# Optimization experiments

Measured on AMD Instinct MI355X. Metric: run time of the kernel, lower is better.

Reference implementation:

```python
import jax, jax.numpy as jnp
import numpy as np

B, S, L = 4, 1024, 512          # batch, max_seqlen, actual per-seq length
H, D = 12, 64                   # heads, head_dim
DIM = H * D                     # 768
NNZ = B * L                     # 2048 unpadded tokens


def setup_inputs() -> dict:
    key = jax.random.key(0)
    k1, k2, k3 = jax.random.split(key, 3)
    hidden_states = jax.random.normal(k1, (NNZ, DIM), jnp.float32)
    Wqkv_w = jax.random.normal(k2, (3 * DIM, DIM), jnp.float32) * 0.02
    Wqkv_b = jnp.zeros((3 * DIM,), jnp.float32)
    # ALiBi-style bias; in the real model it also encodes the padding mask (-inf),
    # here random values suffice for a correctness baseline.
    bias = jax.random.normal(k3, (B, H, S, S), jnp.float32) * 0.1
    # each sequence occupies the first L slots of its row in the padded layout
    indices = (jnp.arange(B)[:, None] * S + jnp.arange(L)[None, :]).reshape(-1).astype(jnp.int32)
    cu_seqlens = (jnp.arange(B + 1) * L).astype(jnp.int32)
    attn_mask = jnp.zeros((B, S), jnp.int32).at[:, :L].set(1)
    return dict(hidden_states=hidden_states, Wqkv_w=Wqkv_w, Wqkv_b=Wqkv_b,
                bias=bias, indices=indices, attn_mask=attn_mask,
                cu_seqlens=cu_seqlens, max_seqlen_in_batch=S)


def reference(hidden_states, Wqkv_w, Wqkv_b, bias, indices, attn_mask,
              cu_seqlens, max_seqlen_in_batch):
    b = attn_mask.shape[0]
    s = max_seqlen_in_batch
    # QKV projection on unpadded tokens: (nnz, 3*dim)
    qkv = hidden_states @ Wqkv_w.T + Wqkv_b
    # pad_input: scatter unpadded rows into (b*s) padded layout
    padded = jnp.zeros((b * s, qkv.shape[-1]), qkv.dtype).at[indices].set(qkv)
    qkv = padded.reshape(b, s, 3, H, D)
    q, k, v = qkv[:, :, 0], qkv[:, :, 1], qkv[:, :, 2]  # (b, s, h, d)
    scale = 1.0 / float(np.sqrt(D))
    scores = jnp.einsum('bqhd,bkhd->bhqk', q, k) * scale + bias  # (b,h,s,s)
    probs = jax.nn.softmax(scores, axis=-1)
    ctx = jnp.einsum('bhqk,bkhd->bqhd', probs, v)  # (b, s, h, d)
    # unpad_input_only: gather back rows where attn_mask == 1 (== indices)
    return ctx.reshape(b * s, H * D)[indices]
```

## Files before the change

kernel.cpp:

```cpp
#include <hip/hip_runtime.h>
#include <hip/hip_bf16.h>
#include <cstdint>

typedef short  s16x8 __attribute__((ext_vector_type(8)));
typedef ushort u16x8 __attribute__((ext_vector_type(8)));
typedef ushort u16x4 __attribute__((ext_vector_type(4)));
typedef float  f32x4 __attribute__((ext_vector_type(4)));

#define B_    4
#define S_    1024
#define H_    12
#define D_    64
#define DIM_  768
#define QSCALE 0.18033688011112042f
#define LOG2E  1.4426950408889634f

#define NTAIL 384
#define NGEMM 576

__device__ __forceinline__ ushort f2bf(float f) {
    __bf16 h = (__bf16)f;
    return __builtin_bit_cast(ushort, h);
}

__device__ __forceinline__ u16x8 cvt8(f32x4 x, f32x4 y) {
    u16x8 r;
    r[0]=f2bf(x[0]); r[1]=f2bf(x[1]); r[2]=f2bf(x[2]); r[3]=f2bf(x[3]);
    r[4]=f2bf(y[0]); r[5]=f2bf(y[1]); r[6]=f2bf(y[2]); r[7]=f2bf(y[3]);
    return r;
}

__global__ __launch_bounds__(256) void gemm_tail(
    const float* __restrict__ hidden, const float* __restrict__ W,
    const float* __restrict__ bvec, const float* __restrict__ bias,
    const int* __restrict__ cu,
    ushort* __restrict__ Qu, ushort* __restrict__ Ku, ushort* __restrict__ Vt,
    float* __restrict__ T, int nrows, int nnz)
{
    const int t = threadIdx.x;

    if ((int)blockIdx.x >= NGEMM) {
        const int blk = blockIdx.x - NGEMM;
        const int w = t >> 6, l = t & 63, grp = l >> 4, lc = l & 15;
        for (int rid = blk*16 + w*4 + grp; rid < nrows; rid += NTAIL*16) {
            const int h = rid / nnz;
            const int u = rid - h * nnz;
            int b = 0;
            while (cu[b+1] <= u) b++;
            const int q  = u - cu[b];
            const int Lb = cu[b+1] - cu[b];
            const float* rp = bias + ((size_t)(b*H_ + h)*S_ + q)*S_;
            float s = 0.0f;
            for (int kbase = Lb; kbase < S_; kbase += 512) {
                f32x4 v[8];
                #pragma unroll
                for (int i = 0; i < 8; i++) {
                    const int k = kbase + lc*4 + i*64;
                    v[i] = (k < S_) ? *(const f32x4*)(rp + k) : (f32x4)(-1e30f);
                }
                #pragma unroll
                for (int i = 0; i < 8; i++)
                    s += exp2f(v[i][0]*LOG2E) + exp2f(v[i][1]*LOG2E)
                       + exp2f(v[i][2]*LOG2E) + exp2f(v[i][3]*LOG2E);
            }
            s += __shfl_xor(s, 1, 64);
            s += __shfl_xor(s, 2, 64);
            s += __shfl_xor(s, 4, 64);
            s += __shfl_xor(s, 8, 64);
            if (lc == 0) T[(size_t)(b*H_ + h)*S_ + q] = s;
        }
        return;
    }

    const int bid = ((int)blockIdx.x % 8) * (NGEMM/8) + (int)blockIdx.x / 8;

    __shared__ ushort As[128][40];
    __shared__ ushort Bs[64][40];

    const int n0 = (bid % 36) * 64;
    const int m0 = (bid / 36) * 128;
    const int w  = t >> 6, l = t & 63, lg = l >> 4, lc = l & 15;

    const int srow = t >> 1, shalf = t & 1;
    const int brow = t >> 2, bq = t & 3;
    const float* aSrc = hidden + (size_t)(m0 + srow) * DIM_ + shalf * 16;
    const float* bSrc = W      + (size_t)(n0 + brow) * DIM_ + bq * 8;

    f32x4 acc[2][4];
    #pragma unroll
    for (int i = 0; i < 2; i++)
        #pragma unroll
        for (int j = 0; j < 4; j++) acc[i][j] = (f32x4)0.0f;

    for (int k0 = 0; k0 < DIM_; k0 += 32) {
        __syncthreads();
        {
            const f32x4* a4 = (const f32x4*)(aSrc + k0);
            f32x4 x0 = a4[0], x1 = a4[1], x2 = a4[2], x3 = a4[3];
            const f32x4* b4 = (const f32x4*)(bSrc + k0);
            f32x4 y0 = b4[0], y1 = b4[1];
            *(u16x8*)&As[srow][shalf*16]     = cvt8(x0, x1);
            *(u16x8*)&As[srow][shalf*16 + 8] = cvt8(x2, x3);
            *(u16x8*)&Bs[brow][bq*8]         = cvt8(y0, y1);
        }
        __syncthreads();
        s16x8 af[2], bfr[4];
        #pragma unroll
        for (int mi = 0; mi < 2; mi++)
            af[mi] = *(const s16x8*)&As[w*32 + mi*16 + lc][lg*8];
        #pragma unroll
        for (int ni = 0; ni < 4; ni++)
            bfr[ni] = *(const s16x8*)&Bs[ni*16 + lc][lg*8];
        #pragma unroll
        for (int mi = 0; mi < 2; mi++)
            #pragma unroll
            for (int ni = 0; ni < 4; ni++)
                acc[mi][ni] = __builtin_amdgcn_mfma_f32_16x16x32_bf16(
                                  af[mi], bfr[ni], acc[mi][ni], 0, 0, 0);
    }

    const int sec = n0 / DIM_;
    float bv[4];
    #pragma unroll
    for (int ni = 0; ni < 4; ni++) bv[ni] = bvec[n0 + ni*16 + lc];

    #pragma unroll
    for (int mi = 0; mi < 2; mi++) {
        const int r = m0 + w*32 + mi*16 + lg*4;
        if (sec == 2) {
            int b = 0;
            while (cu[b+1] <= r) b++;
            const int q = r - cu[b];
            #pragma unroll
            for (int ni = 0; ni < 4; ni++) {
                const int nl = (n0 - 2*DIM_) + ni*16 + lc;
                const int h = nl >> 6, d = nl & 63;
                u16x4 pk;
                #pragma unroll
                for (int j = 0; j < 4; j++) pk[j] = f2bf(acc[mi][ni][j] + bv[ni]);
                *(u16x4*)&Vt[((size_t)((b*H_ + h)*64 + d))*S_ + q] = pk;
            }
        } else {
            #pragma unroll
            for (int j = 0; j < 4; j++) {
                #pragma unroll
                for (int ni = 0; ni < 4; ni++) {
                    const int nl = (n0 - sec*DIM_) + ni*16 + lc;
                    float v = acc[mi][ni][j] + bv[ni];
                    if (sec == 0) Qu[(size_t)(r+j)*DIM_ + nl] = f2bf(v * QSCALE);
                    else          Ku[(size_t)(r+j)*DIM_ + nl] = f2bf(v);
                }
            }
        }
    }
}

__global__ __launch_bounds__(128) void attn_kernel(
    const ushort* __restrict__ Qu, const ushort* __restrict__ Ku,
    const ushort* __restrict__ Vt, const float* __restrict__ bias,
    const float* __restrict__ T, const int* __restrict__ cu,
    float* __restrict__ out)
{
    const int b  = blockIdx.x >> 4, qt = blockIdx.x & 15;
    const int h  = blockIdx.y;
    const int cu0 = cu[b];
    const int Lb  = cu[b+1] - cu0;
    const int qbase = qt * 32;
    if (qbase >= Lb) return;

    const int t = threadIdx.x, w = t >> 6, l = t & 63, lg = l >> 4, lc = l & 15;

    __shared__ ushort Ks[64][72];
    __shared__ ushort Vs[80][72];
    __shared__ ushort Ps[2][16][72];

    for (int i = t; i < 16*9; i += 128) {
        const int row = 64 + i/9, ch = i%9;
        u16x8 v = (u16x8)0;
        if (row == 64 && ch < 8)
            #pragma unroll
            for (int e = 0; e < 8; e++) v[e] = 0x3F80;
        *(u16x8*)&Vs[row][ch*8] = v;
    }

    const float*  bias_b = bias + (size_t)(b*H_ + h)*S_*S_;
    const ushort* kbase  = Ku + (size_t)cu0*DIM_ + h*64;
    const ushort* vbase  = Vt + (size_t)((b*H_ + h)*64)*S_;

    const int krow = t >> 3, kch = t & 7;

    const int rl = w*16 + lg*4;
    int p_[4]; bool val_[4];
    const float* bpr[4];
    #pragma unroll
    for (int j = 0; j < 4; j++) {
        const int r = qbase + rl + j;
        val_[j] = (r < Lb);
        p_[j]   = val_[j] ? r : (Lb - 1);
        bpr[j]  = bias_b + (size_t)p_[j]*S_;
    }

    int qar = qbase + w*16 + lc; if (qar >= Lb) qar = Lb - 1;
    const ushort* qp = Qu + (size_t)(cu0 + qar)*DIM_ + h*64;
    s16x8 qa0 = *(const s16x8*)(qp + lg*8);
    s16x8 qa1 = *(const s16x8*)(qp + 32 + lg*8);

    f32x4 O[4], lsum;
    #pragma unroll
    for (int d = 0; d < 4; d++) O[d] = (f32x4)0.0f;
    lsum = (f32x4)0.0f;

    float pf[4][4];
    u16x8 kr[4], vr[4];
    #pragma unroll
    for (int f = 0; f < 4; f++)
        #pragma unroll
        for (int j = 0; j < 4; j++) pf[f][j] = bpr[j][f*16 + lc];
    #pragma unroll
    for (int i = 0; i < 4; i++) {
        const int r  = krow + i*16;
        const int rc = (r < Lb) ? r : Lb - 1;
        kr[i] = *(const u16x8*)(kbase + (size_t)rc*DIM_ + kch*8);
        vr[i] = *(const u16x8*)(vbase + (size_t)r*S_ + kch*8);
    }

    for (int k0 = 0; k0 < Lb; k0 += 64) {
        __syncthreads();
        #pragma unroll
        for (int i = 0; i < 4; i++) {
            const int r = krow + i*16;
            u16x8 kz = (k0 + r < Lb) ? kr[i] : (u16x8)0;
            *(u16x8*)&Ks[r][kch*8] = kz;
            *(u16x8*)&Vs[r][kch*8] = vr[i];
        }
        __syncthreads();

        f32x4 sc[4];
        #pragma unroll
        for (int f = 0; f < 4; f++)
            #pragma unroll
            for (int j = 0; j < 4; j++) sc[f][j] = pf[f][j] * LOG2E;

        const int kn = k0 + 64;
        if (kn < Lb) {
            #pragma unroll
            for (int f = 0; f < 4; f++)
                #pragma unroll
                for (int j = 0; j < 4; j++) pf[f][j] = bpr[j][kn + f*16 + lc];
            #pragma unroll
            for (int i = 0; i < 4; i++) {
                const int r  = krow + i*16;
                const int rc = (kn + r < Lb) ? kn + r : Lb - 1;
                kr[i] = *(const u16x8*)(kbase + (size_t)rc*DIM_ + kch*8);
                vr[i] = *(const u16x8*)(vbase + (size_t)r*S_ + kn + kch*8);
            }
        }

        #pragma unroll
        for (int f = 0; f < 4; f++) {
            s16x8 kb0 = *(const s16x8*)&Ks[f*16 + lc][lg*8];
            s16x8 kb1 = *(const s16x8*)&Ks[f*16 + lc][32 + lg*8];
            sc[f] = __builtin_amdgcn_mfma_f32_16x16x32_bf16(qa0, kb0, sc[f], 0,0,0);
            sc[f] = __builtin_amdgcn_mfma_f32_16x16x32_bf16(qa1, kb1, sc[f], 0,0,0);
        }
        if (k0 + 64 > Lb) {
            #pragma unroll
            for (int f = 0; f < 4; f++) {
                const int kcol = k0 + f*16 + lc;
                if (kcol >= Lb)
                    #pragma unroll
                    for (int j = 0; j < 4; j++) sc[f][j] = -1e30f;
            }
        }

        #pragma unroll
        for (int f = 0; f < 4; f++)
            #pragma unroll
            for (int j = 0; j < 4; j++)
                Ps[w][lg*4 + j][f*16 + lc] = f2bf(exp2f(sc[f][j]));

        s16x8 pa0 = *(const s16x8*)&Ps[w][lc][lg*8];
        s16x8 pa1 = *(const s16x8*)&Ps[w][lc][32 + lg*8];
        #pragma unroll
        for (int df = 0; df < 4; df++) {
            s16x8 vb0 = *(const s16x8*)&Vs[df*16 + lc][lg*8];
            s16x8 vb1 = *(const s16x8*)&Vs[df*16 + lc][32 + lg*8];
            O[df] = __builtin_amdgcn_mfma_f32_16x16x32_bf16(pa0, vb0, O[df], 0,0,0);
            O[df] = __builtin_amdgcn_mfma_f32_16x16x32_bf16(pa1, vb1, O[df], 0,0,0);
        }
        {
            s16x8 ob0 = *(const s16x8*)&Vs[64 + lc][lg*8];
            s16x8 ob1 = *(const s16x8*)&Vs[64 + lc][32 + lg*8];
            lsum = __builtin_amdgcn_mfma_f32_16x16x32_bf16(pa0, ob0, lsum, 0,0,0);
            lsum = __builtin_amdgcn_mfma_f32_16x16x32_bf16(pa1, ob1, lsum, 0,0,0);
        }
    }

    #pragma unroll
    for (int j = 0; j < 4; j++) {
        float lj = lsum[j] + T[(size_t)(b*H_ + h)*S_ + p_[j]];
        float inv = 1.0f / lj;
        inv = __shfl(inv, l & 48, 64);
        if (val_[j]) {
            float* op = out + (size_t)(cu0 + qbase + rl + j)*DIM_ + h*64;
            #pragma unroll
            for (int df = 0; df < 4; df++) op[df*16 + lc] = O[df][j] * inv;
        }
    }
}

extern "C" void kernel_launch(void* const* d_in, const int* in_sizes, int n_in,
                              void* d_out, int out_size, void* d_ws, size_t ws_size,
                              hipStream_t stream)
{
    const float* hidden  = (const float*)d_in[0];
    const float* W       = (const float*)d_in[1];
    const float* bvec    = (const float*)d_in[2];
    const float* bias    = (const float*)d_in[3];
    const int*   cu      = (const int*)d_in[6];
    float*       out     = (float*)d_out;

    const int NNZ   = in_sizes[0] / DIM_;
    const int nrows = NNZ * H_;

    char* ws = (char*)d_ws;
    const size_t uB  = (size_t)NNZ * DIM_ * 2;
    const size_t vtB = (size_t)B_ * H_ * 64 * S_ * 2;
    ushort* Qu = (ushort*)(ws);
    ushort* Ku = (ushort*)(ws + uB);
    ushort* Vt = (ushort*)(ws + 2*uB);
    float*  T  = (float*)(ws + 2*uB + vtB);

    gemm_tail<<<NGEMM + NTAIL, 256, 0, stream>>>(hidden, W, bvec, bias, cu,
                                                 Qu, Ku, Vt, T, nrows, NNZ);

    dim3 ga(B_*16, H_);
    attn_kernel<<<ga, 128, 0, stream>>>(Qu, Ku, Vt, bias, T, cu, out);
}
```

Baseline: 57.39 us.

## Pre-convert hidden and weights to bf16 in a separate pass before QKV GEMM

Splits the fused GEMM+tail kernel so that a first kernel converts hidden states and Wqkv to bf16 in workspace, alongside the bias tail-sum blocks, and a new GEMM kernel then loads bf16 tiles directly. This removes the repeated fp32 loads and per-tile conversion that the GEMM did for every reused tile, which halves the bytes per GEMM tile load. In exchange it adds a kernel launch, an extra round trip of the converted data through memory, and the GEMM no longer overlaps with the tail blocks.

```diff
diff --git a/kernel.cpp b/kernel.cpp
--- a/kernel.cpp
+++ b/kernel.cpp
@@ -30,17 +30,25 @@
     return r;
 }
 
-__global__ __launch_bounds__(256) void gemm_tail(
+__global__ __launch_bounds__(256) void prep_tail(
     const float* __restrict__ hidden, const float* __restrict__ W,
-    const float* __restrict__ bvec, const float* __restrict__ bias,
-    const int* __restrict__ cu,
-    ushort* __restrict__ Qu, ushort* __restrict__ Ku, ushort* __restrict__ Vt,
-    float* __restrict__ T, int nrows, int nnz)
+    const float* __restrict__ bias, const int* __restrict__ cu,
+    ushort* __restrict__ Ah, ushort* __restrict__ Wh, float* __restrict__ T,
+    int nh, int nw, int ncvt, int nrows, int nnz)
 {
     const int t = threadIdx.x;
-
-    if ((int)blockIdx.x >= NGEMM) {
-        const int blk = blockIdx.x - NGEMM;
+    if ((int)blockIdx.x < ncvt) {
+        const int total = (nh + nw) >> 3;
+        for (int i = blockIdx.x * 256 + t; i < total; i += ncvt * 256) {
+            const float* src; ushort* dst; int off = i << 3;
+            if (off < nh) { src = hidden; dst = Ah; }
+            else          { src = W;      dst = Wh; off -= nh; }
+            f32x4 x0 = *(const f32x4*)(src + off);
+            f32x4 x1 = *(const f32x4*)(src + off + 4);
+            *(u16x8*)(dst + off) = cvt8(x0, x1);
+        }
+    } else {
+        const int blk = blockIdx.x - ncvt;
         const int w = t >> 6, l = t & 63, grp = l >> 4, lc = l & 15;
         for (int rid = blk*16 + w*4 + grp; rid < nrows; rid += NTAIL*16) {
             const int h = rid / nnz;
@@ -69,22 +77,28 @@
             s += __shfl_xor(s, 8, 64);
             if (lc == 0) T[(size_t)(b*H_ + h)*S_ + q] = s;
         }
-        return;
-    }
-
+    }
+}
+
+__global__ __launch_bounds__(256) void qkv_gemm(
+    const ushort* __restrict__ Ah, const ushort* __restrict__ Wh,
+    const float* __restrict__ bvec, const int* __restrict__ cu,
+    ushort* __restrict__ Qu, ushort* __restrict__ Ku, ushort* __restrict__ Vt)
+{
     const int bid = ((int)blockIdx.x % 8) * (NGEMM/8) + (int)blockIdx.x / 8;
 
     __shared__ ushort As[128][40];
     __shared__ ushort Bs[64][40];
 
+    const int t  = threadIdx.x;
     const int n0 = (bid % 36) * 64;
     const int m0 = (bid / 36) * 128;
     const int w  = t >> 6, l = t & 63, lg = l >> 4, lc = l & 15;
 
     const int srow = t >> 1, shalf = t & 1;
     const int brow = t >> 2, bq = t & 3;
-    const float* aSrc = hidden + (size_t)(m0 + srow) * DIM_ + shalf * 16;
-    const float* bSrc = W      + (size_t)(n0 + brow) * DIM_ + bq * 8;
+    const ushort* aSrc = Ah + (size_t)(m0 + srow) * DIM_ + shalf * 16;
+    const ushort* bSrc = Wh + (size_t)(n0 + brow) * DIM_ + bq * 8;
 
     f32x4 acc[2][4];
     #pragma unroll
@@ -94,15 +108,9 @@
 
     for (int k0 = 0; k0 < DIM_; k0 += 32) {
         __syncthreads();
-        {
-            const f32x4* a4 = (const f32x4*)(aSrc + k0);
-            f32x4 x0 = a4[0], x1 = a4[1], x2 = a4[2], x3 = a4[3];
-            const f32x4* b4 = (const f32x4*)(bSrc + k0);
-            f32x4 y0 = b4[0], y1 = b4[1];
-            *(u16x8*)&As[srow][shalf*16]     = cvt8(x0, x1);
-            *(u16x8*)&As[srow][shalf*16 + 8] = cvt8(x2, x3);
-            *(u16x8*)&Bs[brow][bq*8]         = cvt8(y0, y1);
-        }
+        *(u16x8*)&As[srow][shalf*16]     = *(const u16x8*)(aSrc + k0);
+        *(u16x8*)&As[srow][shalf*16 + 8] = *(const u16x8*)(aSrc + k0 + 8);
+        *(u16x8*)&Bs[brow][bq*8]         = *(const u16x8*)(bSrc + k0);
         __syncthreads();
         s16x8 af[2], bfr[4];
         #pragma unroll
@@ -321,6 +329,9 @@
     float*       out     = (float*)d_out;
 
     const int NNZ   = in_sizes[0] / DIM_;
+    const int nh    = NNZ * DIM_;
+    const int nw    = 3 * DIM_ * DIM_;
+    const int ncvt  = (nh + nw) / 8 / 256;
     const int nrows = NNZ * H_;
 
     char* ws = (char*)d_ws;
@@ -330,9 +341,14 @@
     ushort* Ku = (ushort*)(ws + uB);
     ushort* Vt = (ushort*)(ws + 2*uB);
     float*  T  = (float*)(ws + 2*uB + vtB);
-
-    gemm_tail<<<NGEMM + NTAIL, 256, 0, stream>>>(hidden, W, bvec, bias, cu,
-                                                 Qu, Ku, Vt, T, nrows, NNZ);
+    ushort* Ah = (ushort*)(ws + 2*uB + vtB + (size_t)B_*H_*S_*4);
+    ushort* Wh = (ushort*)(ws + 2*uB + vtB + (size_t)B_*H_*S_*4 + (size_t)nh*2);
+
+    prep_tail<<<ncvt + NTAIL, 256, 0, stream>>>(hidden, W, bias, cu,
+                                                Ah, Wh, T, nh, nw, ncvt,
+                                                nrows, NNZ);
+
+    qkv_gemm<<<NGEMM, 256, 0, stream>>>(Ah, Wh, bvec, cu, Qu, Ku, Vt);
 
     dim3 ga(B_*16, H_);
     attn_kernel<<<ga, 128, 0, stream>>>(Qu, Ku, Vt, bias, T, cu, out);
```

New measurement: 60.36 us. 5.2% more time.

## Fuse padded-key bias tail sum into attention kernel, drop tail blocks from GEMM

Applied to the files above, without the earlier changes.

Removes the separate tail-sum blocks from the QKV GEMM launch and instead computes each query row's sum of exp(bias) over the padded key positions inside the attention kernel. The result goes to shared memory instead of a global T buffer. This drops the global write and read of T and shrinks the first kernel's grid. In exchange, the attention blocks now read the padded part of the bias rows themselves before the main loop, which lengthens the critical path of a kernel with only 768 blocks.

```diff
diff --git a/kernel.cpp b/kernel.cpp
--- a/kernel.cpp
+++ b/kernel.cpp
@@ -15,7 +15,6 @@
 #define QSCALE 0.18033688011112042f
 #define LOG2E  1.4426950408889634f
 
-#define NTAIL 384
 #define NGEMM 576
 
 __device__ __forceinline__ ushort f2bf(float f) {
@@ -30,47 +29,12 @@
     return r;
 }
 
-__global__ __launch_bounds__(256) void gemm_tail(
+__global__ __launch_bounds__(256) void qkv_gemm(
     const float* __restrict__ hidden, const float* __restrict__ W,
-    const float* __restrict__ bvec, const float* __restrict__ bias,
-    const int* __restrict__ cu,
-    ushort* __restrict__ Qu, ushort* __restrict__ Ku, ushort* __restrict__ Vt,
-    float* __restrict__ T, int nrows, int nnz)
+    const float* __restrict__ bvec, const int* __restrict__ cu,
+    ushort* __restrict__ Qu, ushort* __restrict__ Ku, ushort* __restrict__ Vt)
 {
     const int t = threadIdx.x;
-
-    if ((int)blockIdx.x >= NGEMM) {
-        const int blk = blockIdx.x - NGEMM;
-        const int w = t >> 6, l = t & 63, grp = l >> 4, lc = l & 15;
-        for (int rid = blk*16 + w*4 + grp; rid < nrows; rid += NTAIL*16) {
-            const int h = rid / nnz;
-            const int u = rid - h * nnz;
-            int b = 0;
-            while (cu[b+1] <= u) b++;
-            const int q  = u - cu[b];
-            const int Lb = cu[b+1] - cu[b];
-            const float* rp = bias + ((size_t)(b*H_ + h)*S_ + q)*S_;
-            float s = 0.0f;
-            for (int kbase = Lb; kbase < S_; kbase += 512) {
-                f32x4 v[8];
-                #pragma unroll
-                for (int i = 0; i < 8; i++) {
-                    const int k = kbase + lc*4 + i*64;
-                    v[i] = (k < S_) ? *(const f32x4*)(rp + k) : (f32x4)(-1e30f);
-                }
-                #pragma unroll
-                for (int i = 0; i < 8; i++)
-                    s += exp2f(v[i][0]*LOG2E) + exp2f(v[i][1]*LOG2E)
-                       + exp2f(v[i][2]*LOG2E) + exp2f(v[i][3]*LOG2E);
-            }
-            s += __shfl_xor(s, 1, 64);
-            s += __shfl_xor(s, 2, 64);
-            s += __shfl_xor(s, 4, 64);
-            s += __shfl_xor(s, 8, 64);
-            if (lc == 0) T[(size_t)(b*H_ + h)*S_ + q] = s;
-        }
-        return;
-    }
 
     const int bid = ((int)blockIdx.x % 8) * (NGEMM/8) + (int)blockIdx.x / 8;
 
@@ -158,8 +122,7 @@
 __global__ __launch_bounds__(128) void attn_kernel(
     const ushort* __restrict__ Qu, const ushort* __restrict__ Ku,
     const ushort* __restrict__ Vt, const float* __restrict__ bias,
-    const float* __restrict__ T, const int* __restrict__ cu,
-    float* __restrict__ out)
+    const int* __restrict__ cu, float* __restrict__ out)
 {
     const int b  = blockIdx.x >> 4, qt = blockIdx.x & 15;
     const int h  = blockIdx.y;
@@ -173,6 +136,7 @@
     __shared__ ushort Ks[64][72];
     __shared__ ushort Vs[80][72];
     __shared__ ushort Ps[2][16][72];
+    __shared__ float  tailS[32];
 
     for (int i = t; i < 16*9; i += 128) {
         const int row = 64 + i/9, ch = i%9;
@@ -224,6 +188,28 @@
         vr[i] = *(const u16x8*)(vbase + (size_t)r*S_ + kch*8);
     }
 
+    {
+        const int trow = t >> 2, tc4 = t & 3;
+        int trq = qbase + trow; if (trq >= Lb) trq = Lb - 1;
+        const float* rp = bias_b + (size_t)trq*S_;
+        float ts = 0.0f;
+        for (int kb = Lb; kb < S_; kb += 128) {
+            f32x4 v[8];
+            #pragma unroll
+            for (int i = 0; i < 8; i++) {
+                const int k = kb + tc4*4 + i*16;
+                v[i] = (k < S_) ? *(const f32x4*)(rp + k) : (f32x4)(-1e30f);
+            }
+            #pragma unroll
+            for (int i = 0; i < 8; i++)
+                ts += exp2f(v[i][0]*LOG2E) + exp2f(v[i][1]*LOG2E)
+                    + exp2f(v[i][2]*LOG2E) + exp2f(v[i][3]*LOG2E);
+        }
+        ts += __shfl_xor(ts, 1, 64);
+        ts += __shfl_xor(ts, 2, 64);
+        if (tc4 == 0) tailS[trow] = ts;
+    }
+
     for (int k0 = 0; k0 < Lb; k0 += 64) {
         __syncthreads();
         #pragma unroll
@@ -298,7 +284,7 @@
 
     #pragma unroll
     for (int j = 0; j < 4; j++) {
-        float lj = lsum[j] + T[(size_t)(b*H_ + h)*S_ + p_[j]];
+        float lj = lsum[j] + tailS[rl + j];
         float inv = 1.0f / lj;
         inv = __shfl(inv, l & 48, 64);
         if (val_[j]) {
@@ -320,20 +306,16 @@
     const int*   cu      = (const int*)d_in[6];
     float*       out     = (float*)d_out;
 
-    const int NNZ   = in_sizes[0] / DIM_;
-    const int nrows = NNZ * H_;
+    const int NNZ = in_sizes[0] / DIM_;
 
     char* ws = (char*)d_ws;
-    const size_t uB  = (size_t)NNZ * DIM_ * 2;
-    const size_t vtB = (size_t)B_ * H_ * 64 * S_ * 2;
+    const size_t uB = (size_t)NNZ * DIM_ * 2;
     ushort* Qu = (ushort*)(ws);
     ushort* Ku = (ushort*)(ws + uB);
     ushort* Vt = (ushort*)(ws + 2*uB);
-    float*  T  = (float*)(ws + 2*uB + vtB);
-
-    gemm_tail<<<NGEMM + NTAIL, 256, 0, stream>>>(hidden, W, bvec, bias, cu,
-                                                 Qu, Ku, Vt, T, nrows, NNZ);
+
+    qkv_gemm<<<NGEMM, 256, 0, stream>>>(hidden, W, bvec, cu, Qu, Ku, Vt);
 
     dim3 ga(B_*16, H_);
-    attn_kernel<<<ga, 128, 0, stream>>>(Qu, Ku, Vt, bias, T, cu, out);
-}
+    attn_kernel<<<ga, 128, 0, stream>>>(Qu, Ku, Vt, bias, cu, out);
+}
```

Result: slower. 60.92 us (+6.1%).
